# Performance work log

Measured on AMD Instinct MI355X. Metric: run time of the kernel, lower is better.

Reference implementation:

```python
import jax, jax.numpy as jnp
import numpy as np

N_EMBD = 1024
N_HEAD = 16
B, T = 4, 2048


def setup_inputs() -> dict:
    key = jax.random.key(0)
    k1, k2, k3, k4, k5 = jax.random.split(key, 5)
    s = 0.02
    return {
        "x": jax.random.normal(k1, (B, T, N_EMBD), dtype=jnp.float32),
        "w_attn": jax.random.normal(k2, (N_EMBD, 3 * N_EMBD), dtype=jnp.float32) * s,
        "b_attn": jnp.zeros((3 * N_EMBD,), dtype=jnp.float32),
        "w_proj": jax.random.normal(k3, (N_EMBD, N_EMBD), dtype=jnp.float32) * s,
        "b_proj": jnp.zeros((N_EMBD,), dtype=jnp.float32),
    }


def reference(x, w_attn, b_attn, w_proj, b_proj):
    Bb, Tt, C = x.shape
    hd = C // N_HEAD  # head dim
    qkv = x @ w_attn + b_attn                      # [B,T,3C]
    q, k, v = jnp.split(qkv, 3, axis=-1)
    # [B,T,C] -> [B,H,T,hd]
    def heads(t):
        return t.reshape(Bb, Tt, N_HEAD, hd).transpose(0, 2, 1, 3)
    q, k, v = heads(q), heads(k), heads(v)
    scale = 1.0 / np.sqrt(hd).astype(np.float32)
    attn = jnp.einsum("bhqd,bhkd->bhqk", q, k) * scale  # [B,H,T,T]
    causal = jnp.tril(jnp.ones((Tt, Tt), dtype=bool))
    attn = jnp.where(causal, attn, -jnp.inf)
    attn = jax.nn.softmax(attn, axis=-1)
    y = jnp.einsum("bhqk,bhkd->bhqd", attn, v)          # [B,H,T,hd]
    y = y.transpose(0, 2, 1, 3).reshape(Bb, Tt, C)
    return y @ w_proj + b_proj
```

## Files before the change

kernel.cpp:

```cpp
#include <hip/hip_runtime.h>
#include <cmath>


typedef short short8 __attribute__((ext_vector_type(8)));
typedef short short4v __attribute__((ext_vector_type(4)));
typedef float f32x4 __attribute__((ext_vector_type(4)));

__device__ __forceinline__ short f2bf(float f) {
  unsigned u = __builtin_bit_cast(unsigned, f);
  u = (u + 0x7fffu + ((u >> 16) & 1u)) >> 16;
  return (short)u;
}

__device__ __forceinline__ float exp2_fast(float x) {
  float r;
  asm("v_exp_f32 %0, %1" : "=v"(r) : "v"(x));
  return r;
}

__device__ __forceinline__ void gld_lds16(const void* g, void* l) {
  __builtin_amdgcn_global_load_lds(
      (__attribute__((address_space(1))) void*)g,
      (__attribute__((address_space(3))) void*)l,
      16, 0, 0);
}

__global__ void cast_bf16_kernel(const float* __restrict__ in,
                                 short* __restrict__ out, int n4) {
  int i = blockIdx.x * blockDim.x + threadIdx.x;
  if (i < n4) {
    const float4 v = ((const float4*)in)[i];
    short4v o;
    o.x = f2bf(v.x); o.y = f2bf(v.y); o.z = f2bf(v.z); o.w = f2bf(v.w);
    ((short4v*)out)[i] = o;
  }
}

__global__ void transpose_cast_kernel(const float* __restrict__ in,
                                      short* __restrict__ out, int R, int C) {
  __shared__ float tile[32][33];
  int c0 = blockIdx.x * 32, r0 = blockIdx.y * 32;
  int tx = threadIdx.x & 31, tg = threadIdx.x >> 5;
#pragma unroll
  for (int i = 0; i < 4; ++i) {
    int r = tg * 4 + i;
    tile[r][tx] = in[(size_t)(r0 + r) * C + c0 + tx];
  }
  __syncthreads();
#pragma unroll
  for (int i = 0; i < 4; ++i) {
    int c = tg * 4 + i;
    out[(size_t)(c0 + c) * R + r0 + tx] = f2bf(tile[tx][c]);
  }
}

template <int MODE>
__global__ __launch_bounds__(256) void gemm_bt_kernel(
    const short* __restrict__ A, const short* __restrict__ Bt,
    const float* __restrict__ bias, float* __restrict__ outf,
    short* __restrict__ oq, short* __restrict__ ok, short* __restrict__ ovt,
    int M, int N, int K) {
  __shared__ short lds[16384];
  short* As = lds;
  short* Bs = lds + 8192;
  const int m0 = blockIdx.y * 128, n0 = blockIdx.x * 128;
  const int lane = threadIdx.x & 63, wave = threadIdx.x >> 6;
  const int quad = lane >> 4, l16 = lane & 15;
  const int wm = (wave >> 1) * 64, wn = (wave & 1) * 64;

  const int row_off = lane >> 3;
  const int segsw = ((lane & 7) ^ row_off) * 8;
  const short* Ag = A + (size_t)(m0 + wave * 32 + row_off) * K + segsw;
  const short* Bg = Bt + (size_t)(n0 + wave * 32 + row_off) * K + segsw;

  f32x4 acc[4][4] = {};

  for (int k0 = 0; k0 < K; k0 += 64) {
#pragma unroll
    for (int g = 0; g < 4; ++g) {
      gld_lds16(Ag + (size_t)(g * 8) * K + k0, &As[(wave * 32 + g * 8) * 64]);
      gld_lds16(Bg + (size_t)(g * 8) * K + k0, &Bs[(wave * 32 + g * 8) * 64]);
    }
    __syncthreads();
#pragma unroll
    for (int kh = 0; kh < 2; ++kh) {
      short8 a[4], b[4];
#pragma unroll
      for (int t = 0; t < 4; ++t) {
        const int R = wm + t * 16 + l16;
        a[t] = *(const short8*)&As[R * 64 + (((kh * 4 + quad) ^ (R & 7)) * 8)];
      }
#pragma unroll
      for (int t = 0; t < 4; ++t) {
        const int R = wn + t * 16 + l16;
        b[t] = *(const short8*)&Bs[R * 64 + (((kh * 4 + quad) ^ (R & 7)) * 8)];
      }
#pragma unroll
      for (int mt = 0; mt < 4; ++mt)
#pragma unroll
        for (int nt = 0; nt < 4; ++nt)
          acc[mt][nt] = __builtin_amdgcn_mfma_f32_16x16x32_bf16(
              a[mt], b[nt], acc[mt][nt], 0, 0, 0);
    }
    __syncthreads();
  }

  float bv[4];
#pragma unroll
  for (int nt = 0; nt < 4; ++nt) bv[nt] = bias[n0 + wn + nt * 16 + l16];

  if (MODE == 1) {
#pragma unroll
    for (int mt = 0; mt < 4; ++mt)
#pragma unroll
      for (int nt = 0; nt < 4; ++nt) {
        const int n = n0 + wn + nt * 16 + l16;
#pragma unroll
        for (int r = 0; r < 4; ++r) {
          const int m = m0 + wm + mt * 16 + quad * 4 + r;
          outf[(size_t)m * N + n] = acc[mt][nt][r] + bv[nt];
        }
      }
  } else {
    const int sec = n0 >> 10;
    const int h0 = (n0 & 1023) >> 6;
    const float scale = (sec == 0) ? 0.18033688f : 1.0f;
    short* Cs = lds;
    const int tid = threadIdx.x;
#pragma unroll 1
    for (int p = 0; p < 2; ++p) {
      if ((wave >> 1) == p) {
#pragma unroll
        for (int mt = 0; mt < 4; ++mt)
#pragma unroll
          for (int nt = 0; nt < 4; ++nt) {
            const int col = wn + nt * 16 + l16;
#pragma unroll
            for (int r = 0; r < 4; ++r) {
              const int row = mt * 16 + quad * 4 + r;
              const short hv = f2bf((acc[mt][nt][r] + bv[nt]) * scale);
              if (sec == 2) Cs[col * 72 + row] = hv;
              else          Cs[row * 136 + col] = hv;
            }
          }
      }
      __syncthreads();
      if (sec < 2) {
        short* dst = (sec == 0) ? oq : ok;
        const int rw = tid >> 2, seg = tid & 3;
        const int m = m0 + p * 64 + rw, b_ = m >> 11, tt = m & 2047;
        const short* sp = &Cs[rw * 136 + seg * 32];
        short* gp = dst +
            ((size_t)(b_ * 16 + h0 + (seg >> 1)) * 2048 + tt) * 64 +
            (seg & 1) * 32;
#pragma unroll
        for (int i = 0; i < 4; ++i) ((short8*)gp)[i] = ((const short8*)sp)[i];
      } else {
        const int b_ = m0 >> 11, t0 = m0 & 2047;
        const int col = tid >> 1, rh = tid & 1;
        const int bh = b_ * 16 + h0 + (col >> 6), d = col & 63;
        const short* sp = &Cs[col * 72 + rh * 32];
        short* gp = ovt + ((size_t)bh * 64 + d) * 2048 + t0 + p * 64 + rh * 32;
#pragma unroll
        for (int i = 0; i < 4; ++i) ((short8*)gp)[i] = ((const short8*)sp)[i];
      }
      __syncthreads();
    }
  }
}

__global__ __launch_bounds__(256, 6) void attn_kernel(
    const short* __restrict__ q, const short* __restrict__ k,
    const short* __restrict__ vt, short* __restrict__ y) {
  __shared__ short Ks[64 * 64];
  __shared__ short Vs[64 * 64];
  __shared__ short Ps[4][16 * 72];
  const int lane = threadIdx.x & 63, wave = threadIdx.x >> 6;
  const int quad = lane >> 4, l16 = lane & 15;
  const int g = blockIdx.x;
  const int bh = g & 63;
  const int j = 31 - (g >> 6);
  const int b_ = bh >> 4, h = bh & 15;
  const int q0 = j * 64 + wave * 16;

  const short* qbh = q + (size_t)bh * 2048 * 64;
  const short* kbh = k + (size_t)bh * 2048 * 64;
  const short* vbh = vt + (size_t)bh * 64 * 2048;
  short* Pw = Ps[wave];

  const short8 qf0 = *(const short8*)&qbh[(q0 + l16) * 64 + quad * 8];
  const short8 qf1 = *(const short8*)&qbh[(q0 + l16) * 64 + 32 + quad * 8];

  short8 ones;
#pragma unroll
  for (int i = 0; i < 8; ++i) ones[i] = (short)0x3F80;

  f32x4 O[4] = {};
  f32x4 lacc = {};

  const int srow = lane >> 3;
  const int scol = ((lane & 7) ^ srow) * 8;
  const int r0s = wave * 16;

#pragma unroll 1
  for (int c = 0; c <= j; ++c) {
    const int kt0 = c * 64;
    gld_lds16(kbh + (size_t)(kt0 + r0s + srow) * 64 + scol, &Ks[r0s * 64]);
    gld_lds16(kbh + (size_t)(kt0 + r0s + 8 + srow) * 64 + scol, &Ks[(r0s + 8) * 64]);
    gld_lds16(vbh + (size_t)(r0s + srow) * 2048 + kt0 + scol, &Vs[r0s * 64]);
    gld_lds16(vbh + (size_t)(r0s + 8 + srow) * 2048 + kt0 + scol, &Vs[(r0s + 8) * 64]);
    __syncthreads();

    const int sw = l16 & 7;
    f32x4 sc4[4];
#pragma unroll
    for (int cf = 0; cf < 4; ++cf) {
      const int row = cf * 16 + l16;
      const short8 kfa = *(const short8*)&Ks[row * 64 + ((quad ^ sw) * 8)];
      const short8 kfb = *(const short8*)&Ks[row * 64 + (((quad + 4) ^ sw) * 8)];
      f32x4 z = {};
      z = __builtin_amdgcn_mfma_f32_16x16x32_bf16(qf0, kfa, z, 0, 0, 0);
      z = __builtin_amdgcn_mfma_f32_16x16x32_bf16(qf1, kfb, z, 0, 0, 0);
      sc4[cf] = z;
    }

    if (c == j) {
#pragma unroll
      for (int cf = 0; cf < 4; ++cf) {
        const int col = kt0 + cf * 16 + l16;
#pragma unroll
        for (int r = 0; r < 4; ++r) {
          const int rowg = q0 + quad * 4 + r;
          float e = exp2_fast(sc4[cf][r]);
          e = (col > rowg) ? 0.f : e;
          Pw[(quad * 4 + r) * 72 + cf * 16 + l16] = f2bf(e);
        }
      }
    } else {
#pragma unroll
      for (int cf = 0; cf < 4; ++cf)
#pragma unroll
        for (int r = 0; r < 4; ++r)
          Pw[(quad * 4 + r) * 72 + cf * 16 + l16] = f2bf(exp2_fast(sc4[cf][r]));
    }
    asm volatile("s_waitcnt lgkmcnt(0)" ::: "memory");
    const short8 pf0 = *(const short8*)&Pw[l16 * 72 + quad * 8];
    const short8 pf1 = *(const short8*)&Pw[l16 * 72 + 32 + quad * 8];

    lacc = __builtin_amdgcn_mfma_f32_16x16x32_bf16(pf0, ones, lacc, 0, 0, 0);
    lacc = __builtin_amdgcn_mfma_f32_16x16x32_bf16(pf1, ones, lacc, 0, 0, 0);

#pragma unroll
    for (int dt = 0; dt < 4; ++dt) {
      const int d = dt * 16 + l16;
      const short8 vf0 = *(const short8*)&Vs[d * 64 + ((quad ^ sw) * 8)];
      const short8 vf1 = *(const short8*)&Vs[d * 64 + (((quad + 4) ^ sw) * 8)];
      O[dt] = __builtin_amdgcn_mfma_f32_16x16x32_bf16(pf0, vf0, O[dt], 0, 0, 0);
      O[dt] = __builtin_amdgcn_mfma_f32_16x16x32_bf16(pf1, vf1, O[dt], 0, 0, 0);
    }
    __syncthreads();
  }

  float inv[4];
#pragma unroll
  for (int r = 0; r < 4; ++r) inv[r] = 1.0f / lacc[r];
#pragma unroll
  for (int dt = 0; dt < 4; ++dt) {
    const int d = dt * 16 + l16;
#pragma unroll
    for (int r = 0; r < 4; ++r) {
      const int t_ = q0 + quad * 4 + r;
      y[((size_t)b_ * 2048 + t_) * 1024 + h * 64 + d] = f2bf(O[dt][r] * inv[r]);
    }
  }
}

extern "C" void kernel_launch(void* const* d_in, const int* in_sizes, int n_in,
                              void* d_out, int out_size, void* d_ws, size_t ws_size,
                              hipStream_t stream) {
  const float* x      = (const float*)d_in[0];
  const float* w_attn = (const float*)d_in[1];
  const float* b_attn = (const float*)d_in[2];
  const float* w_proj = (const float*)d_in[3];
  const float* b_proj = (const float*)d_in[4];
  float* out = (float*)d_out;

  short* xb  = (short*)d_ws;
  short* wTa = xb + (size_t)8192 * 1024;
  short* wTp = wTa + (size_t)3072 * 1024;
  short* qb  = wTp + (size_t)1024 * 1024;
  short* kb  = qb + (size_t)64 * 2048 * 64;
  short* vtb = kb + (size_t)64 * 2048 * 64;
  short* yb  = vtb + (size_t)64 * 2048 * 64;

  cast_bf16_kernel<<<8192, 256, 0, stream>>>(x, xb, 8192 * 1024 / 4);
  transpose_cast_kernel<<<dim3(96, 32), 256, 0, stream>>>(w_attn, wTa, 1024, 3072);
  transpose_cast_kernel<<<dim3(32, 32), 256, 0, stream>>>(w_proj, wTp, 1024, 1024);

  gemm_bt_kernel<0><<<dim3(24, 64), 256, 0, stream>>>(
      xb, wTa, b_attn, nullptr, qb, kb, vtb, 8192, 3072, 1024);

  attn_kernel<<<2048, 256, 0, stream>>>(qb, kb, vtb, yb);

  gemm_bt_kernel<1><<<dim3(8, 64), 256, 0, stream>>>(
      yb, wTp, b_proj, out, nullptr, nullptr, nullptr, 8192, 1024, 1024);
}
```

Measured before the change: 262.9 us.

## Replace QKV GEMM with 256x256-tile, 8-wave, double-buffered pipelined kernel

Adds a dedicated QKV projection kernel that uses 256x256 output tiles with 512 threads, 128 KB of dynamic LDS for double buffering, staggered global-to-LDS prefetch interleaved with MFMA phases, s_setprio around the MFMA bursts, and a swizzled block order to improve L2 reuse. The epilogue writes Q/K in head layout and V transposed, staged through LDS. The goal is more data reuse per loaded tile and overlap of loads with compute. In exchange it raises register and LDS pressure and lowers occupancy, and it launches fewer blocks (384) than the device has CUs times two, which risks tail imbalance.

```diff
diff --git a/kernel.cpp b/kernel.cpp
--- a/kernel.cpp
+++ b/kernel.cpp
@@ -23,6 +23,12 @@
       (__attribute__((address_space(1))) void*)g,
       (__attribute__((address_space(3))) void*)l,
       16, 0, 0);
+}
+
+__device__ __forceinline__ void barx() {
+  asm volatile("" ::: "memory");
+  __builtin_amdgcn_s_barrier();
+  asm volatile("" ::: "memory");
 }
 
 __global__ void cast_bf16_kernel(const float* __restrict__ in,
@@ -54,15 +60,185 @@
   }
 }
 
+
+#define LDA(mp)                                                              \
+  _Pragma("unroll") for (int i_ = 0; i_ < 2; ++i_) {                         \
+    const int R_ = wm2 * 128 + ((mp) + i_) * 16 + l16;                       \
+    _Pragma("unroll") for (int kh_ = 0; kh_ < 2; ++kh_)                      \
+        a[i_][kh_] = *(const short8*)&Abuf[R_ * 64 +                         \
+                         (((kh_ * 4 + quad) ^ (R_ & 7)) * 8)];               \
+  }
+
+#define DOMFMA(mp)                                                           \
+  __builtin_amdgcn_s_setprio(1);                                             \
+  _Pragma("unroll") for (int i_ = 0; i_ < 2; ++i_)                           \
+  _Pragma("unroll") for (int n_ = 0; n_ < 4; ++n_)                           \
+  _Pragma("unroll") for (int kh_ = 0; kh_ < 2; ++kh_)                        \
+      acc[(mp) + i_][n_] = __builtin_amdgcn_mfma_f32_16x16x32_bf16(          \
+          a[i_][kh_], b[n_][kh_], acc[(mp) + i_][n_], 0, 0, 0);              \
+  __builtin_amdgcn_s_setprio(0);
+
+__global__ __launch_bounds__(512, 2) void qkv_gemm_kernel(
+    const short* __restrict__ A, const short* __restrict__ Bt,
+    const float* __restrict__ bias,
+    short* __restrict__ oq, short* __restrict__ ok, short* __restrict__ ovt,
+    int M, int N, int K) {
+  extern __shared__ short lds[];
+  const int NT = K >> 6;
+  const int lane = threadIdx.x & 63, wave = threadIdx.x >> 6;
+  const int quad = lane >> 4, l16 = lane & 15;
+  const int wm2 = wave >> 2, wn4 = wave & 3;
+
+  const int nbn = N >> 8;
+  const int swz = (blockIdx.x & 7) * ((int)gridDim.x >> 3) + (blockIdx.x >> 3);
+  const int m0 = (swz / nbn) * 256, n0 = (swz % nbn) * 256;
+
+  const int r8 = lane >> 3;
+  const int sw8 = ((lane & 7) ^ r8) * 8;
+  const short* Ab0 = A + (size_t)(m0 + wave * 8 + r8) * K + sw8;
+  const short* Bb0 = Bt + (size_t)(n0 + wave * 8 + r8) * K + sw8;
+  short* ldsw = lds + wave * 512;
+
+  auto stage = [&](int t, int mat, int rA, int rB) {
+    const short* g = (mat ? Bb0 : Ab0) + t * 64;
+    short* d = ldsw + (t & 1) * 32768 + mat * 16384;
+    gld_lds16(g + (size_t)rA * K, d + rA * 64);
+    gld_lds16(g + (size_t)rB * K, d + rB * 64);
+  };
+
+  f32x4 acc[8][4] = {};
+
+  stage(0, 1, 0, 64);
+  stage(0, 1, 128, 192);
+  stage(0, 0, 0, 128);
+  stage(0, 0, 64, 192);
+  stage(1, 1, 0, 64);
+  stage(1, 1, 128, 192);
+  stage(1, 0, 0, 128);
+  asm volatile("s_waitcnt vmcnt(6)" ::: "memory");
+  barx();
+
+#pragma unroll 1
+  for (int t = 0; t < NT; ++t) {
+    const short* Abuf = lds + (t & 1) * 32768;
+    const short* Bbuf = Abuf + 16384;
+    short8 b[4][2], a[2][2];
+
+#pragma unroll
+    for (int n_ = 0; n_ < 4; ++n_) {
+      const int R_ = wn4 * 64 + n_ * 16 + l16;
+#pragma unroll
+      for (int kh_ = 0; kh_ < 2; ++kh_)
+        b[n_][kh_] = *(const short8*)&Bbuf[R_ * 64 +
+                         (((kh_ * 4 + quad) ^ (R_ & 7)) * 8)];
+    }
+    LDA(0)
+    if (t + 1 < NT) stage(t + 1, 0, 64, 192);
+    barx();
+    asm volatile("s_waitcnt lgkmcnt(0)" ::: "memory");
+    DOMFMA(0)
+    barx();
+
+    LDA(2)
+    if (t + 2 < NT) stage(t + 2, 1, 0, 64);
+    barx();
+    asm volatile("s_waitcnt lgkmcnt(0)" ::: "memory");
+    DOMFMA(2)
+    barx();
+
+    LDA(4)
+    if (t + 2 < NT) stage(t + 2, 1, 128, 192);
+    barx();
+    asm volatile("s_waitcnt lgkmcnt(0)" ::: "memory");
+    DOMFMA(4)
+    barx();
+
+    LDA(6)
+    if (t + 2 < NT) stage(t + 2, 0, 0, 128);
+    barx();
+    asm volatile("s_waitcnt lgkmcnt(0)" ::: "memory");
+    DOMFMA(6)
+    if (t == NT - 2)
+      asm volatile("s_waitcnt vmcnt(0)" ::: "memory");
+    else
+      asm volatile("s_waitcnt vmcnt(6)" ::: "memory");
+    barx();
+  }
+
+  const int sec = n0 >> 10;
+  const int h0 = (n0 & 1023) >> 6;
+  const float scale = (sec == 0) ? 0.18033688f : 1.0f;
+  float bv[4];
+#pragma unroll
+  for (int n_ = 0; n_ < 4; ++n_) bv[n_] = bias[n0 + wn4 * 64 + n_ * 16 + l16];
+  const int b_ = m0 >> 11, t0 = m0 & 2047;
+
+  if (sec < 2) {
+    short* dst = (sec == 0) ? oq : ok;
+#pragma unroll 1
+    for (int p = 0; p < 2; ++p) {
+      if (wm2 == p) {
+#pragma unroll
+        for (int mt = 0; mt < 8; ++mt)
+#pragma unroll
+          for (int n_ = 0; n_ < 4; ++n_) {
+            const int col = wn4 * 64 + n_ * 16 + l16;
+#pragma unroll
+            for (int r = 0; r < 4; ++r)
+              lds[(mt * 16 + quad * 4 + r) * 264 + col] =
+                  f2bf((acc[mt][n_][r] + bv[n_]) * scale);
+          }
+      }
+      __syncthreads();
+      const int hl = wave & 3, rg = wave >> 2;
+      const short* sp = &lds[(rg * 64 + r8) * 264 + hl * 64 + (lane & 7) * 8];
+      short* gp = dst +
+          ((size_t)(b_ * 16 + h0 + hl) * 2048 + t0 + p * 128 + rg * 64 + r8) * 64 +
+          (lane & 7) * 8;
+#pragma unroll
+      for (int i = 0; i < 8; ++i)
+        *(short8*)(gp + (size_t)i * 512) = *(const short8*)(sp + i * 8 * 264);
+      __syncthreads();
+    }
+  } else {
+#pragma unroll 1
+    for (int p = 0; p < 2; ++p) {
+      if (wm2 == p) {
+#pragma unroll
+        for (int mt = 0; mt < 8; ++mt)
+#pragma unroll
+          for (int n_ = 0; n_ < 4; ++n_) {
+            const int col = wn4 * 64 + n_ * 16 + l16;
+#pragma unroll
+            for (int r = 0; r < 4; ++r)
+              lds[col * 136 + mt * 16 + quad * 4 + r] =
+                  f2bf(acc[mt][n_][r] + bv[n_]);
+          }
+      }
+      __syncthreads();
+      const int cw = wave * 32 + (lane >> 4);
+#pragma unroll
+      for (int i = 0; i < 8; ++i) {
+        const int c = cw + i * 4;
+        const int bh = b_ * 16 + h0 + (c >> 6), d = c & 63;
+        *(short8*)(ovt + ((size_t)bh * 64 + d) * 2048 + t0 + p * 128 +
+                   (lane & 15) * 8) =
+            *(const short8*)&lds[c * 136 + (lane & 15) * 8];
+      }
+      __syncthreads();
+    }
+  }
+}
+
 template <int MODE>
 __global__ __launch_bounds__(256) void gemm_bt_kernel(
     const short* __restrict__ A, const short* __restrict__ Bt,
     const float* __restrict__ bias, float* __restrict__ outf,
     short* __restrict__ oq, short* __restrict__ ok, short* __restrict__ ovt,
     int M, int N, int K) {
-  __shared__ short lds[16384];
-  short* As = lds;
-  short* Bs = lds + 8192;
+  __shared__ short slds[16384];
+  short* As = slds;
+  short* Bs = slds + 8192;
   const int m0 = blockIdx.y * 128, n0 = blockIdx.x * 128;
   const int lane = threadIdx.x & 63, wave = threadIdx.x >> 6;
   const int quad = lane >> 4, l16 = lane & 15;
@@ -121,51 +297,6 @@
           outf[(size_t)m * N + n] = acc[mt][nt][r] + bv[nt];
         }
       }
-  } else {
-    const int sec = n0 >> 10;
-    const int h0 = (n0 & 1023) >> 6;
-    const float scale = (sec == 0) ? 0.18033688f : 1.0f;
-    short* Cs = lds;
-    const int tid = threadIdx.x;
-#pragma unroll 1
-    for (int p = 0; p < 2; ++p) {
-      if ((wave >> 1) == p) {
-#pragma unroll
-        for (int mt = 0; mt < 4; ++mt)
-#pragma unroll
-          for (int nt = 0; nt < 4; ++nt) {
-            const int col = wn + nt * 16 + l16;
-#pragma unroll
-            for (int r = 0; r < 4; ++r) {
-              const int row = mt * 16 + quad * 4 + r;
-              const short hv = f2bf((acc[mt][nt][r] + bv[nt]) * scale);
-              if (sec == 2) Cs[col * 72 + row] = hv;
-              else          Cs[row * 136 + col] = hv;
-            }
-          }
-      }
-      __syncthreads();
-      if (sec < 2) {
-        short* dst = (sec == 0) ? oq : ok;
-        const int rw = tid >> 2, seg = tid & 3;
-        const int m = m0 + p * 64 + rw, b_ = m >> 11, tt = m & 2047;
-        const short* sp = &Cs[rw * 136 + seg * 32];
-        short* gp = dst +
-            ((size_t)(b_ * 16 + h0 + (seg >> 1)) * 2048 + tt) * 64 +
-            (seg & 1) * 32;
-#pragma unroll
-        for (int i = 0; i < 4; ++i) ((short8*)gp)[i] = ((const short8*)sp)[i];
-      } else {
-        const int b_ = m0 >> 11, t0 = m0 & 2047;
-        const int col = tid >> 1, rh = tid & 1;
-        const int bh = b_ * 16 + h0 + (col >> 6), d = col & 63;
-        const short* sp = &Cs[col * 72 + rh * 32];
-        short* gp = ovt + ((size_t)bh * 64 + d) * 2048 + t0 + p * 64 + rh * 32;
-#pragma unroll
-        for (int i = 0; i < 4; ++i) ((short8*)gp)[i] = ((const short8*)sp)[i];
-      }
-      __syncthreads();
-    }
   }
 }
 
@@ -293,12 +424,20 @@
   short* vtb = kb + (size_t)64 * 2048 * 64;
   short* yb  = vtb + (size_t)64 * 2048 * 64;
 
+  static int lds_attr_done = 0;
+  if (!lds_attr_done) {
+    (void)hipFuncSetAttribute(reinterpret_cast<const void*>(qkv_gemm_kernel),
+                              hipFuncAttributeMaxDynamicSharedMemorySize,
+                              131072);
+    lds_attr_done = 1;
+  }
+
   cast_bf16_kernel<<<8192, 256, 0, stream>>>(x, xb, 8192 * 1024 / 4);
   transpose_cast_kernel<<<dim3(96, 32), 256, 0, stream>>>(w_attn, wTa, 1024, 3072);
   transpose_cast_kernel<<<dim3(32, 32), 256, 0, stream>>>(w_proj, wTp, 1024, 1024);
 
-  gemm_bt_kernel<0><<<dim3(24, 64), 256, 0, stream>>>(
-      xb, wTa, b_attn, nullptr, qb, kb, vtb, 8192, 3072, 1024);
+  qkv_gemm_kernel<<<384, 512, 131072, stream>>>(
+      xb, wTa, b_attn, qb, kb, vtb, 8192, 3072, 1024);
 
   attn_kernel<<<2048, 256, 0, stream>>>(qb, kb, vtb, yb);
 
```

Measured after the change: 249.4 us. -5.1%, faster.
